# Kernel tuning notes

Hardware: AMD Instinct MI355X
Metric: run time of the kernel (lower is better)

## Reference

```python
import jax, jax.numpy as jnp
import numpy as np

NUM_FREQS = 10
NUM_VOXELS = 512
N_POINTS = 262144
IN_DIM = 3
INPUT_CH = IN_DIM + 2 * NUM_FREQS * IN_DIM  # 63


def posenc(x, num_freqs):
    # NeRF positional encoding: [x, sin(x*2^0), cos(x*2^0), ..., sin(x*2^(F-1)), cos(x*2^(F-1))]
    freqs = (2.0 ** jnp.arange(num_freqs)).astype(x.dtype)           # (F,)
    xf = x[:, None, :] * freqs[None, :, None]                        # (N, F, D)
    sc = jnp.stack([jnp.sin(xf), jnp.cos(xf)], axis=2)               # (N, F, 2, D)
    return jnp.concatenate([x, sc.reshape(x.shape[0], -1)], axis=-1)  # (N, D + 2*F*D)


def setup_inputs() -> dict:
    key = jax.random.key(0)
    k_x, k_w, k_v = jax.random.split(key, 3)
    X = jax.random.normal(k_x, (N_POINTS, IN_DIM), dtype=jnp.float32)
    # linear_mappings reshaped to (3*num_voxels, input_ch), used as Linear weight (no bias)
    W = jax.random.normal(k_w, (3 * NUM_VOXELS, INPUT_CH), dtype=jnp.float32) * 0.02
    row_ids = jnp.arange(N_POINTS, dtype=jnp.int64 if jax.config.jax_enable_x64 else jnp.int32)
    voxel_ids = jax.random.randint(k_v, (N_POINTS,), 0, NUM_VOXELS)
    return {"X": X, "W": W, "row_ids": row_ids, "voxel_ids": voxel_ids}


def reference(X, W, row_ids, voxel_ids):
    encoded_X = posenc(X, NUM_FREQS)                      # (N, 63)
    rgb_clusters = encoded_X @ W.T                        # (N, 3*num_voxels) -- wasteful dense GEMM
    # col_indices per selected row: [3v, 3v+1, 3v+2]
    cols = jnp.stack([3 * voxel_ids, 3 * voxel_ids + 1, 3 * voxel_ids + 2], axis=1)  # (M, 3)
    vals = rgb_clusters[row_ids[:, None], cols]           # (M, 3)
    rgb = jnp.zeros((X.shape[0], 3), dtype=X.dtype)
    rgb = rgb.at[row_ids].set(vals)
    return rgb
```

## Files before the change

kernel.cpp:

```cpp
#include <hip/hip_runtime.h>
#include <math.h>

#define N_POINTS   262144
#define NUM_FREQS  10
#define NUM_VOXELS 512
#define HALF_VOX   256
#define VSTRIDE    200
#define W_FLOATS_PER_HALF (HALF_VOX * 189)


typedef _Float16 half2v __attribute__((ext_vector_type(2)));

__device__ __forceinline__ half2v u2h(unsigned int u) {
    union { unsigned int u; half2v h; } c; c.u = u; return c.h;
}

__device__ __forceinline__ float dot2acc(half2v a, half2v b, float acc) {
#if __has_builtin(__builtin_amdgcn_fdot2)
    return __builtin_amdgcn_fdot2(a, b, acc, false);
#else
    return acc + (float)a[0] * (float)b[0] + (float)a[1] * (float)b[1];
#endif
}

__device__ __forceinline__ half2v pkrtz(float a, float b) {
#if __has_builtin(__builtin_amdgcn_cvt_pkrtz)
    auto r = __builtin_amdgcn_cvt_pkrtz(a, b);
    union { decltype(r) r_; half2v h; } c; c.r_ = r; return c.h;
#else
    half2v h; h[0] = (_Float16)a; h[1] = (_Float16)b; return h;
#endif
}

__global__ __launch_bounds__(1024) void voxlin_lds(
    const float* __restrict__ X,
    const float* __restrict__ W,
    const int* __restrict__ row_ids,
    const int* __restrict__ voxel_ids,
    float* __restrict__ out)
{
    __shared__ _Float16 lw[HALF_VOX * VSTRIDE];

    const int t = threadIdx.x;
    const int i = blockIdx.x * 1024 + t;

    const int   v  = voxel_ids[i];
    const float x0 = X[3*i + 0];
    const float x1 = X[3*i + 1];
    const float x2 = X[3*i + 2];
    const int   r  = row_ids[i];

    half2v eh[32];
    eh[0] = pkrtz(x0, x1);
    eh[1] = pkrtz(x2, 0.0f);
    {
        float s0, c0, s1, c1, s2, c2;
        __sincosf(x0, &s0, &c0);
        __sincosf(x1, &s1, &c1);
        __sincosf(x2, &s2, &c2);
        #pragma unroll
        for (int f = 0; f < NUM_FREQS; ++f) {
            const int b = 2 + 3 * f;
            eh[b + 0] = pkrtz(s0, s1);
            eh[b + 1] = pkrtz(s2, c0);
            eh[b + 2] = pkrtz(c1, c2);
            if (f < NUM_FREQS - 1) {
                const float ns0 = 2.0f*s0*c0, nc0 = c0*c0 - s0*s0;
                const float ns1 = 2.0f*s1*c1, nc1 = c1*c1 - s1*s1;
                const float ns2 = 2.0f*s2*c2, nc2 = c2*c2 - s2*s2;
                s0 = ns0; c0 = nc0; s1 = ns1; c1 = nc1; s2 = ns2; c2 = nc2;
            }
        }
    }

    float a0 = 0.0f, a1 = 0.0f, a2 = 0.0f;

    #pragma unroll
    for (int h = 0; h < 2; ++h) {
        const float* __restrict__ Wh = W + h * W_FLOATS_PER_HALF;
        for (int idx = t; idx < W_FLOATS_PER_HALF; idx += 1024) {
            const float wv  = Wh[idx];
            const int   lv  = idx / 189;
            const int   e   = idx - lv * 189;
            const int   row = e / 63;
            const int   col = e - row * 63;
            const int   pc  = col + (col >= 3);
            lw[lv * VSTRIDE + row * 64 + pc] = (_Float16)wv;
        }
        if (t < HALF_VOX * 11) {
            const int lv = t / 11, s = t - lv * 11;
            const int off = (s == 0) ? 3 : (s == 1) ? 67 : (s == 2) ? 131
                                                        : (189 + s);
            lw[lv * VSTRIDE + off] = (_Float16)0.0f;
        }
        __syncthreads();

        if ((v >> 8) == h) {
            const uint4* __restrict__ wb =
                (const uint4*)lw + (v & (HALF_VOX - 1)) * 25;
            float acc[3];
            #pragma unroll
            for (int rr = 0; rr < 3; ++rr) {
                float a = 0.0f;
                #pragma unroll
                for (int k = 0; k < 8; ++k) {
                    const uint4 q = wb[rr * 8 + k];
                    a = dot2acc(u2h(q.x), eh[4*k + 0], a);
                    a = dot2acc(u2h(q.y), eh[4*k + 1], a);
                    a = dot2acc(u2h(q.z), eh[4*k + 2], a);
                    a = dot2acc(u2h(q.w), eh[4*k + 3], a);
                }
                acc[rr] = a;
            }
            a0 = acc[0]; a1 = acc[1]; a2 = acc[2];
        }
        __syncthreads();
    }

    out[3*r + 0] = a0;
    out[3*r + 1] = a1;
    out[3*r + 2] = a2;
}

extern "C" void kernel_launch(void* const* d_in, const int* in_sizes, int n_in,
                              void* d_out, int out_size, void* d_ws, size_t ws_size,
                              hipStream_t stream) {
    const float* X         = (const float*)d_in[0];
    const float* W         = (const float*)d_in[1];
    const int*   row_ids   = (const int*)d_in[2];
    const int*   voxel_ids = (const int*)d_in[3];
    float*       out       = (float*)d_out;
    (void)d_ws; (void)ws_size;

    voxlin_lds<<<N_POINTS / 1024, 1024, 0, stream>>>(X, W, row_ids, voxel_ids, out);
}
```

Baseline: 81.97 us.

## Pre-pack weights to padded fp16 layout in a separate kernel, copy to LDS with float4

Adds a small pack kernel that converts W once per call into the padded fp16 per-voxel layout the main kernel expects, written to the workspace. Each of the 256 main-kernel blocks then fills LDS with plain vectorized float4 copies instead of scalar loads with div/mod index math and fp32-to-fp16 conversion. This removes redundant per-block repacking work but adds an extra kernel launch and a dependency through global memory. A scalar fp32 fallback kernel is used if the workspace is too small.

```diff
diff --git a/kernel.cpp b/kernel.cpp
--- a/kernel.cpp
+++ b/kernel.cpp
@@ -6,7 +6,8 @@
 #define NUM_VOXELS 512
 #define HALF_VOX   256
 #define VSTRIDE    200
-#define W_FLOATS_PER_HALF (HALF_VOX * 189)
+#define HALF_HALFS (HALF_VOX * VSTRIDE)
+#define HALF_F4    (HALF_HALFS / 8)
 
 
 typedef _Float16 half2v __attribute__((ext_vector_type(2)));
@@ -32,14 +33,40 @@
 #endif
 }
 
+__global__ __launch_bounds__(1024) void pack_w(
+    const float* __restrict__ W, _Float16* __restrict__ Wp)
+{
+    const int g  = blockIdx.x * 1024 + threadIdx.x;
+    const int v  = g / 50;
+    const int p0 = (g - v * 50) * 4;
+    union { _Float16 h[4]; float2 f2; } u;
+    #pragma unroll
+    for (int j = 0; j < 4; ++j) {
+        const int p = p0 + j;
+        float val = 0.0f;
+        if (p < 192) {
+            const int row = p >> 6, col = p & 63;
+            if (col != 3) {
+                const int wc = col - (col >= 4);
+                val = W[v * 189 + row * 63 + wc];
+            }
+        }
+        u.h[j] = (_Float16)val;
+    }
+    _Float16* dst = Wp + (size_t)(v >> 8) * HALF_HALFS
+                       + (size_t)(v & 255) * VSTRIDE + p0;
+    *reinterpret_cast<float2*>(dst) = u.f2;
+}
+
 __global__ __launch_bounds__(1024) void voxlin_lds(
     const float* __restrict__ X,
-    const float* __restrict__ W,
+    const _Float16* __restrict__ Wp,
     const int* __restrict__ row_ids,
     const int* __restrict__ voxel_ids,
     float* __restrict__ out)
 {
-    __shared__ _Float16 lw[HALF_VOX * VSTRIDE];
+    __shared__ float4 lwv[HALF_F4];
+    _Float16* const lw = (_Float16*)lwv;
 
     const int t = threadIdx.x;
     const int i = blockIdx.x * 1024 + t;
@@ -77,27 +104,15 @@
 
     #pragma unroll
     for (int h = 0; h < 2; ++h) {
-        const float* __restrict__ Wh = W + h * W_FLOATS_PER_HALF;
-        for (int idx = t; idx < W_FLOATS_PER_HALF; idx += 1024) {
-            const float wv  = Wh[idx];
-            const int   lv  = idx / 189;
-            const int   e   = idx - lv * 189;
-            const int   row = e / 63;
-            const int   col = e - row * 63;
-            const int   pc  = col + (col >= 3);
-            lw[lv * VSTRIDE + row * 64 + pc] = (_Float16)wv;
-        }
-        if (t < HALF_VOX * 11) {
-            const int lv = t / 11, s = t - lv * 11;
-            const int off = (s == 0) ? 3 : (s == 1) ? 67 : (s == 2) ? 131
-                                                        : (189 + s);
-            lw[lv * VSTRIDE + off] = (_Float16)0.0f;
-        }
+        const float4* __restrict__ src = (const float4*)Wp + h * HALF_F4;
+        #pragma unroll
+        for (int j = t; j < HALF_F4; j += 1024)
+            lwv[j] = src[j];
         __syncthreads();
 
         if ((v >> 8) == h) {
             const uint4* __restrict__ wb =
-                (const uint4*)lw + (v & (HALF_VOX - 1)) * 25;
+                (const uint4*)lw + (v & (HALF_VOX - 1)) * (VSTRIDE / 8);
             float acc[3];
             #pragma unroll
             for (int rr = 0; rr < 3; ++rr) {
@@ -122,6 +137,40 @@
     out[3*r + 2] = a2;
 }
 
+__global__ __launch_bounds__(256) void voxlin_fallback(
+    const float* __restrict__ X, const float* __restrict__ W,
+    const int* __restrict__ row_ids, const int* __restrict__ voxel_ids,
+    float* __restrict__ out)
+{
+    const int i = blockIdx.x * 256 + threadIdx.x;
+    if (i >= N_POINTS) return;
+    const float x0 = X[3*i], x1 = X[3*i+1], x2 = X[3*i+2];
+    const int v = voxel_ids[i];
+    const float* __restrict__ w0 = W + v * 189;
+    const float* __restrict__ w1 = w0 + 63;
+    const float* __restrict__ w2 = w0 + 126;
+    float a0 = x0*w0[0] + x1*w0[1] + x2*w0[2];
+    float a1 = x0*w1[0] + x1*w1[1] + x2*w1[2];
+    float a2 = x0*w2[0] + x1*w2[1] + x2*w2[2];
+    float s0, c0, s1, c1, s2, c2;
+    __sincosf(x0, &s0, &c0); __sincosf(x1, &s1, &c1); __sincosf(x2, &s2, &c2);
+    #pragma unroll
+    for (int f = 0; f < NUM_FREQS; ++f) {
+        const int b = 3 + 6*f;
+        a0 += s0*w0[b] + s1*w0[b+1] + s2*w0[b+2] + c0*w0[b+3] + c1*w0[b+4] + c2*w0[b+5];
+        a1 += s0*w1[b] + s1*w1[b+1] + s2*w1[b+2] + c0*w1[b+3] + c1*w1[b+4] + c2*w1[b+5];
+        a2 += s0*w2[b] + s1*w2[b+1] + s2*w2[b+2] + c0*w2[b+3] + c1*w2[b+4] + c2*w2[b+5];
+        if (f < NUM_FREQS - 1) {
+            const float ns0 = 2.0f*s0*c0, nc0 = c0*c0 - s0*s0;
+            const float ns1 = 2.0f*s1*c1, nc1 = c1*c1 - s1*s1;
+            const float ns2 = 2.0f*s2*c2, nc2 = c2*c2 - s2*s2;
+            s0 = ns0; c0 = nc0; s1 = ns1; c1 = nc1; s2 = ns2; c2 = nc2;
+        }
+    }
+    const int rr = row_ids[i];
+    out[3*rr] = a0; out[3*rr+1] = a1; out[3*rr+2] = a2;
+}
+
 extern "C" void kernel_launch(void* const* d_in, const int* in_sizes, int n_in,
                               void* d_out, int out_size, void* d_ws, size_t ws_size,
                               hipStream_t stream) {
@@ -130,7 +179,16 @@
     const int*   row_ids   = (const int*)d_in[2];
     const int*   voxel_ids = (const int*)d_in[3];
     float*       out       = (float*)d_out;
-    (void)d_ws; (void)ws_size;
 
-    voxlin_lds<<<N_POINTS / 1024, 1024, 0, stream>>>(X, W, row_ids, voxel_ids, out);
+    const size_t need = (size_t)2 * HALF_HALFS * sizeof(_Float16);
+
+    if (ws_size >= need) {
+        _Float16* Wp = (_Float16*)d_ws;
+        pack_w<<<50, 1024, 0, stream>>>(W, Wp);
+        voxlin_lds<<<N_POINTS / 1024, 1024, 0, stream>>>(X, Wp, row_ids,
+                                                         voxel_ids, out);
+    } else {
+        voxlin_fallback<<<(N_POINTS + 255) / 256, 256, 0, stream>>>(
+            X, W, row_ids, voxel_ids, out);
+    }
 }
```

Result: faster. 69.55 us (-15.2%).
